# Performance work log

Hardware: AMD Instinct MI355X
Metric: run time of the kernel (lower is better)

## Reference

```python
import jax, jax.numpy as jnp
import numpy as np

N, D, H = 4096, 1024, 8
DH = D // H
EPS = 1e-5


def layer_norm(x, g, b):
    mu = jnp.mean(x, axis=-1, keepdims=True)
    var = jnp.mean(jnp.square(x - mu), axis=-1, keepdims=True)
    return (x - mu) * jax.lax.rsqrt(var + EPS) * g + b


def setup_inputs() -> dict:
    key = jax.random.key(0)
    ks = jax.random.split(key, 12)
    s = 0.02
    inp = {
        "x": jax.random.normal(ks[0], (N, D), dtype=jnp.float32),
        "adj": (jax.random.uniform(ks[1], (N, N)) < 0.01).astype(jnp.float32),
        "Wq": jax.random.normal(ks[2], (D, D), dtype=jnp.float32) * s,
        "Wk": jax.random.normal(ks[3], (D, D), dtype=jnp.float32) * s,
        "Wv": jax.random.normal(ks[4], (D, D), dtype=jnp.float32) * s,
        "Wo_w": jax.random.normal(ks[5], (D, D), dtype=jnp.float32) * s,
        "Wo_b": jnp.zeros((D,), dtype=jnp.float32),
        "adj_bias": jnp.full((H,), 1.0, dtype=jnp.float32),
        "ln1_g": jnp.ones((D,), dtype=jnp.float32),
        "ln1_b": jnp.zeros((D,), dtype=jnp.float32),
        "ffn_ln_g": jnp.ones((D,), dtype=jnp.float32),
        "ffn_ln_b": jnp.zeros((D,), dtype=jnp.float32),
        "ffn_w1": jax.random.normal(ks[6], (D, 2 * D), dtype=jnp.float32) * s,
        "ffn_b1": jnp.zeros((2 * D,), dtype=jnp.float32),
        "ffn_w2": jax.random.normal(ks[7], (2 * D, D), dtype=jnp.float32) * s,
        "ffn_b2": jnp.zeros((D,), dtype=jnp.float32),
    }
    return inp


def reference(x, adj, Wq, Wk, Wv, Wo_w, Wo_b, adj_bias, ln1_g, ln1_b,
              ffn_ln_g, ffn_ln_b, ffn_w1, ffn_b1, ffn_w2, ffn_b2):
    scale = DH ** -0.5
    Q = (x @ Wq).reshape(N, H, DH)
    K = (x @ Wk).reshape(N, H, DH)
    V = (x @ Wv).reshape(N, H, DH)
    # attn[i,h,j] = <Q_i, K_j> * scale + beta_h * adj[i,j]
    attn = jnp.einsum('bhd,nhd->bhn', Q, K) * scale
    attn = attn + adj_bias[None, :, None] * adj[:, None, :]
    attn = jax.nn.softmax(attn, axis=-1)  # dropout in eval mode -> identity
    out = jnp.einsum('bhn,nhd->bhd', attn, V).reshape(N, D)
    out = out @ Wo_w + Wo_b
    h = layer_norm(x + out, ln1_g, ln1_b)
    f = layer_norm(h, ffn_ln_g, ffn_ln_b)
    f = jax.nn.gelu(f @ ffn_w1 + ffn_b1, approximate=False) @ ffn_w2 + ffn_b2
    return h + f
```

## Files before the change

kernel.cpp:

```cpp
#include <hip/hip_runtime.h>
#include <hip/hip_bf16.h>
#include <cstdint>
#include <cstddef>

typedef __hip_bfloat16 bf16;
typedef __attribute__((ext_vector_type(8))) short short8;
typedef __attribute__((ext_vector_type(4))) short short4v;
typedef __attribute__((ext_vector_type(4))) float floatx4;
typedef unsigned long long u64;

#define DEVI static __device__ __forceinline__

DEVI void load_lds16(const void* g, void* l) {
  __builtin_amdgcn_global_load_lds((const __attribute__((address_space(1))) unsigned int*)g,
                                   (__attribute__((address_space(3))) unsigned int*)l, 16, 0, 0);
}
DEVI short8 ld8(const bf16* p) { return *(const short8*)p; }
DEVI floatx4 mfma16(short8 a, short8 b, floatx4 c) {
  return __builtin_amdgcn_mfma_f32_16x16x32_bf16(a, b, c, 0, 0, 0);
}
DEVI short bfb(float f) { bf16 h = __float2bfloat16(f); return __builtin_bit_cast(short, h); }
DEVI float fbf(short s) { bf16 h = __builtin_bit_cast(bf16, s); return __bfloat162float(h); }

__global__ __launch_bounds__(256)
void prep_kernel(const float* __restrict__ x, bf16* __restrict__ xb,
                 const float* __restrict__ adj, u64* __restrict__ bits) {
  const int row = blockIdx.x, tid = threadIdx.x;
  const int wave = tid >> 6, lane = tid & 63;
  float4 v = ((const float4*)(x + (size_t)row * 1024))[tid];
  bf16* o = xb + (size_t)row * 1024 + tid * 4;
  o[0] = __float2bfloat16(v.x); o[1] = __float2bfloat16(v.y);
  o[2] = __float2bfloat16(v.z); o[3] = __float2bfloat16(v.w);
  const float* arow = adj + (size_t)row * 4096;
#pragma unroll
  for (int it = 0; it < 16; it++) {
    int col = it * 256 + tid;
    u64 m = __ballot(arow[col] != 0.f);
    if (lane == 0) bits[(size_t)row * 64 + it * 4 + wave] = m;
  }
}

DEVI void tr_tile(const float* in, bf16* out, int R, int C, int bx, int by) {
  __shared__ float t[32][33];
  int c0 = bx * 32, r0 = by * 32;
  int tx = threadIdx.x, ty = threadIdx.y;
#pragma unroll
  for (int i = 0; i < 32; i += 8) t[ty + i][tx] = in[(size_t)(r0 + ty + i) * C + c0 + tx];
  __syncthreads();
#pragma unroll
  for (int i = 0; i < 32; i += 8)
    out[(size_t)(c0 + ty + i) * R + r0 + tx] = __float2bfloat16(t[tx][ty + i]);
}

__global__ __launch_bounds__(256)
void tr_all(const float* Wq, const float* Wk, const float* Wv, const float* Wo,
            const float* W1, const float* W2,
            bf16* Wqkvt, bf16* Wot, bf16* W1t, bf16* W2t) {
  int id = blockIdx.x;
  if (id < 4096) {
    int w = id >> 10, t = id & 1023;
    const float* in = w == 0 ? Wq : w == 1 ? Wk : w == 2 ? Wv : Wo;
    bf16* out = w == 0 ? Wqkvt : w == 1 ? Wqkvt + 1024ull * 1024
                : w == 2 ? Wqkvt + 2048ull * 1024 : Wot;
    tr_tile(in, out, 1024, 1024, t & 31, t >> 5);
  } else if (id < 6144) {
    int t = id - 4096;
    tr_tile(W1, W1t, 1024, 2048, t & 63, t >> 6);
  } else {
    int t = id - 6144;
    tr_tile(W2, W2t, 2048, 1024, t & 31, t >> 5);
  }
}

__global__ __launch_bounds__(256)
void tr_bf16p(const bf16* __restrict__ in, bf16* __restrict__ out, int inLd) {
  __shared__ bf16 t[32][33];
  int c0 = blockIdx.x * 32, r0 = blockIdx.y * 32;
  int tx = threadIdx.x, ty = threadIdx.y;
#pragma unroll
  for (int i = 0; i < 32; i += 8) t[ty + i][tx] = in[(size_t)(r0 + ty + i) * inLd + c0 + tx];
  __syncthreads();
#pragma unroll
  for (int i = 0; i < 32; i += 8) {
    int k = r0 + tx;
    int pk = (k & ~63) | ((k & 15) << 2) | ((k >> 4) & 3);
    out[(size_t)(c0 + ty + i) * 4096 + pk] = t[tx][ty + i];
  }
}

template <int MODE>
__global__ __launch_bounds__(256)
void gemm_bt(const bf16* __restrict__ A, const bf16* __restrict__ Bt,
             const float* __restrict__ bias, const float* __restrict__ resid,
             float* __restrict__ outF, bf16* __restrict__ outB,
             int M, int Nn, int K) {
  __shared__ alignas(16) bf16 As[3][128 * 32];
  __shared__ alignas(16) bf16 Bs[3][128 * 32];
  const int tid = threadIdx.x;
  const int wave = tid >> 6, lane = tid & 63;
  const int m0 = blockIdx.y * 128, n0 = blockIdx.x * 128;
  const int wr = (wave >> 1) * 64, wc = (wave & 1) * 64;
  const int l15 = lane & 15, qq = lane >> 4;
  const int lr = lane >> 2, l4 = lane & 3;
  const int Kspan = K / gridDim.z;
  const int kbeg = blockIdx.z * Kspan;
  const int T = Kspan >> 5;

  floatx4 acc[4][4];
#pragma unroll
  for (int i = 0; i < 4; i++)
#pragma unroll
    for (int j = 0; j < 4; j++) acc[i][j] = (floatx4)0.f;

  const bf16* gA0 = A + (size_t)(m0 + wave * 16 + lr) * K + kbeg + l4 * 8;
  const bf16* gA1 = gA0 + (size_t)64 * K;
  const bf16* gB0 = Bt + (size_t)(n0 + wave * 16 + lr) * K + kbeg + l4 * 8;
  const bf16* gB1 = gB0 + (size_t)64 * K;
  const int lo = wave * 16 * 32;

  auto stage = [&](int t, int buf) {
    int kt = t * 32;
    load_lds16(gA0 + kt, &As[buf][lo]);
    load_lds16(gA1 + kt, &As[buf][64 * 32 + lo]);
    load_lds16(gB0 + kt, &Bs[buf][lo]);
    load_lds16(gB1 + kt, &Bs[buf][64 * 32 + lo]);
  };
  stage(0, 0);
  stage(1, 1);

  int bc = 0;
  for (int t = 0; t < T; ++t) {
    if (t < T - 1) asm volatile("s_waitcnt vmcnt(4) lgkmcnt(0)" ::: "memory");
    else           asm volatile("s_waitcnt vmcnt(0) lgkmcnt(0)" ::: "memory");
    __builtin_amdgcn_s_barrier();
    if (t + 2 < T) { int bs = bc == 0 ? 2 : bc - 1; stage(t + 2, bs); }

    short8 af[4], bfr[4];
#pragma unroll
    for (int mi = 0; mi < 4; mi++) af[mi] = ld8(&As[bc][(wr + mi * 16 + l15) * 32 + qq * 8]);
#pragma unroll
    for (int ni = 0; ni < 4; ni++) bfr[ni] = ld8(&Bs[bc][(wc + ni * 16 + l15) * 32 + qq * 8]);
#pragma unroll
    for (int mi = 0; mi < 4; mi++)
#pragma unroll
      for (int ni = 0; ni < 4; ni++)
        acc[mi][ni] = mfma16(af[mi], bfr[ni], acc[mi][ni]);
    bc = bc == 2 ? 0 : bc + 1;
  }

  const size_t zoff = (size_t)blockIdx.z * M * Nn;
#pragma unroll
  for (int mi = 0; mi < 4; mi++) {
    int row = m0 + wr + mi * 16 + qq * 4;
#pragma unroll
    for (int ni = 0; ni < 4; ni++) {
      int col = n0 + wc + ni * 16 + l15;
      float bv = 0.f;
      if (MODE == 2) bv = bias[col];
      if (MODE == 4 && blockIdx.z == 0) bv = bias[col];
#pragma unroll
      for (int r = 0; r < 4; r++) {
        float v = acc[mi][ni][r] + bv;
        size_t off = (size_t)(row + r) * Nn + col;
        if (MODE == 0) {
          outB[off] = __float2bfloat16(v);
        } else if (MODE == 2) {
          outB[off] = __float2bfloat16(0.5f * v * (1.f + erff(v * 0.70710678118654752f)));
        } else {
          if (resid && blockIdx.z == 1) v += resid[off];
          outF[zoff + off] = v;
        }
      }
    }
  }
}

__global__ __launch_bounds__(256, 3)
void attn_kernel(const bf16* __restrict__ QKV, const bf16* __restrict__ Vtp,
                 const u64* __restrict__ adjbits, const float* __restrict__ adj_bias,
                 bf16* __restrict__ AOpart, float* __restrict__ lpart) {
  __shared__ alignas(16) bf16 Kf[16 * 512];
  __shared__ alignas(16) bf16 Vf[16 * 512];
  __shared__ alignas(16) bf16 Ps[4][32 * 68];
  const int q0 = blockIdx.x * 128;
  const int h = blockIdx.y;
  const int split = blockIdx.z;
  const int k0 = split * 1024;
  const int tid = threadIdx.x, wave = tid >> 6, lane = tid & 63;
  const int l15 = lane & 15, qq = lane >> 4;
  const float beta = adj_bias[h];
  const float scale = 0.08838834764831845f;

  short8 qf[2][4];
#pragma unroll
  for (int mi = 0; mi < 2; mi++)
#pragma unroll
    for (int kk = 0; kk < 4; kk++)
      qf[mi][kk] = ld8(&QKV[(size_t)(q0 + wave * 32 + mi * 16 + l15) * 3072 +
                            h * 128 + kk * 32 + qq * 8]);

  floatx4 o[2][8];
#pragma unroll
  for (int mi = 0; mi < 2; mi++)
#pragma unroll
    for (int ni = 0; ni < 8; ni++) o[mi][ni] = (floatx4)0.f;
  float lrow[2][4];
#pragma unroll
  for (int mi = 0; mi < 2; mi++)
#pragma unroll
    for (int r = 0; r < 4; r++) lrow[mi][r] = 0.f;

  bf16* PsW = &Ps[wave][0];

  short8 kpre[4], vpre[4];
  u64 abc[2][4], abn[2][4];
  auto fetchK = [&](int kt, short8* dst) {
#pragma unroll
    for (int i = 0; i < 4; i++) {
      int fi = wave * 4 + i, ni = fi >> 2, kk = fi & 3;
      dst[i] = ld8(&QKV[(size_t)(kt + ni * 16 + l15) * 3072 + 1024 +
                        h * 128 + kk * 32 + qq * 8]);
    }
  };
  auto fetchV = [&](int kt, short8* dst) {
#pragma unroll
    for (int i = 0; i < 4; i++) {
      int fi = wave * 4 + i, ni = fi >> 1, kk = fi & 1;
      dst[i] = ld8(&Vtp[(size_t)(h * 128 + ni * 16 + l15) * 4096 + kt + kk * 32 + qq * 8]);
    }
  };
  auto fetchA = [&](int t, u64 (*ab)[4]) {
#pragma unroll
    for (int mi = 0; mi < 2; mi++)
#pragma unroll
      for (int r = 0; r < 4; r++)
        ab[mi][r] = adjbits[(size_t)(q0 + wave * 32 + mi * 16 + qq * 4 + r) * 64 +
                            split * 16 + t];
  };
  fetchK(k0, kpre);
  fetchV(k0, vpre);
  fetchA(0, abc);

  for (int t = 0; t < 16; t++) {
    const int kt = k0 + t * 64;
    __syncthreads();
#pragma unroll
    for (int i = 0; i < 4; i++) {
      *(short8*)&Kf[(wave * 4 + i) * 512 + lane * 8] = kpre[i];
      *(short8*)&Vf[(wave * 4 + i) * 512 + lane * 8] = vpre[i];
    }
    __syncthreads();
    if (t < 15) { fetchK(kt + 64, kpre); fetchV(kt + 64, vpre); fetchA(t + 1, abn); }

#pragma unroll
    for (int mi = 0; mi < 2; mi++) {
      floatx4 s[4];
#pragma unroll
      for (int ni = 0; ni < 4; ni++) s[ni] = (floatx4)0.f;
#pragma unroll
      for (int kk = 0; kk < 4; kk++) {
#pragma unroll
        for (int ni = 0; ni < 4; ni++) {
          short8 kf = ld8(&Kf[(ni * 4 + kk) * 512 + lane * 8]);
          s[ni] = mfma16(qf[mi][kk], kf, s[ni]);
        }
      }
#pragma unroll
      for (int r = 0; r < 4; r++) {
        u64 bits = abc[mi][r];
        unsigned lo = (unsigned)(bits >> l15);
        unsigned hi = (unsigned)(bits >> (l15 + 32));
        float b0 = (lo & 1u) ? beta : 0.f;
        float b1 = (lo & 0x10000u) ? beta : 0.f;
        float b2 = (hi & 1u) ? beta : 0.f;
        float b3 = (hi & 0x10000u) ? beta : 0.f;
        float p0 = __expf(fmaf(s[0][r], scale, b0));
        float p1 = __expf(fmaf(s[1][r], scale, b1));
        float p2 = __expf(fmaf(s[2][r], scale, b2));
        float p3 = __expf(fmaf(s[3][r], scale, b3));
        lrow[mi][r] += (p0 + p1) + (p2 + p3);
        short4v pk;
        pk.x = bfb(p0); pk.y = bfb(p1); pk.z = bfb(p2); pk.w = bfb(p3);
        *(short4v*)&PsW[(mi * 16 + qq * 4 + r) * 68 + l15 * 4] = pk;
      }
    }

#pragma unroll
    for (int kk = 0; kk < 2; kk++) {
      short8 af0 = ld8(&PsW[(0 + l15) * 68 + kk * 32 + qq * 8]);
      short8 af1 = ld8(&PsW[(16 + l15) * 68 + kk * 32 + qq * 8]);
#pragma unroll
      for (int ni = 0; ni < 8; ni++) {
        short8 vf = ld8(&Vf[(ni * 2 + kk) * 512 + lane * 8]);
        o[0][ni] = mfma16(af0, vf, o[0][ni]);
        o[1][ni] = mfma16(af1, vf, o[1][ni]);
      }
    }
#pragma unroll
    for (int mi = 0; mi < 2; mi++)
#pragma unroll
      for (int r = 0; r < 4; r++) abc[mi][r] = abn[mi][r];
  }

#pragma unroll
  for (int mi = 0; mi < 2; mi++) {
#pragma unroll
    for (int r = 0; r < 4; r++) {
      float v = lrow[mi][r];
#pragma unroll
      for (int ofs = 1; ofs < 16; ofs <<= 1) v += __shfl_xor(v, ofs, 16);
      int rloc = wave * 32 + mi * 16 + qq * 4 + r;
      int grow = q0 + rloc;
      if (l15 == 0) lpart[((size_t)split * 4096 + grow) * 8 + h] = v;
      bf16* dst = AOpart + ((size_t)split * 4096 + grow) * 1024 + h * 128;
#pragma unroll
      for (int ni = 0; ni < 8; ni++) dst[ni * 16 + l15] = __float2bfloat16(o[mi][ni][r]);
    }
  }
}

__global__ __launch_bounds__(256)
void attn_norm(const bf16* __restrict__ AOpart, const float* __restrict__ lpart,
               bf16* __restrict__ AO) {
  int row = blockIdx.x, tid = threadIdx.x;
  int h = tid >> 5;
  float ls = 0.f;
#pragma unroll
  for (int s = 0; s < 4; s++) ls += lpart[((size_t)s * 4096 + row) * 8 + h];
  float a0 = 0.f, a1 = 0.f, a2 = 0.f, a3 = 0.f;
#pragma unroll
  for (int s = 0; s < 4; s++) {
    short4v v = *(const short4v*)&AOpart[((size_t)s * 4096 + row) * 1024 + tid * 4];
    a0 += fbf(v.x); a1 += fbf(v.y); a2 += fbf(v.z); a3 += fbf(v.w);
  }
  float inv = 1.f / ls;
  bf16* op = AO + (size_t)row * 1024 + tid * 4;
  op[0] = __float2bfloat16(a0 * inv);
  op[1] = __float2bfloat16(a1 * inv);
  op[2] = __float2bfloat16(a2 * inv);
  op[3] = __float2bfloat16(a3 * inv);
}

DEVI void block_sum2(float& a, float& b, float* red) {
#pragma unroll
  for (int o = 1; o < 64; o <<= 1) { a += __shfl_xor(a, o, 64); b += __shfl_xor(b, o, 64); }
  int wv = threadIdx.x >> 6;
  if ((threadIdx.x & 63) == 0) { red[wv] = a; red[4 + wv] = b; }
  __syncthreads();
  a = red[0] + red[1] + red[2] + red[3];
  b = red[4] + red[5] + red[6] + red[7];
  __syncthreads();
}

__global__ __launch_bounds__(256)
void ln2_kernel(const float* __restrict__ x, const float* __restrict__ ao0,
                const float* __restrict__ ao1,
                const float* __restrict__ g1, const float* __restrict__ b1,
                const float* __restrict__ g2, const float* __restrict__ b2,
                float* __restrict__ hout, bf16* __restrict__ fln) {
  __shared__ float red[8];
  const int row = blockIdx.x, tid = threadIdx.x;
  float4 xv = ((const float4*)(x + (size_t)row * 1024))[tid];
  float4 av = ((const float4*)(ao0 + (size_t)row * 1024))[tid];
  float4 aw = ((const float4*)(ao1 + (size_t)row * 1024))[tid];
  float s0 = xv.x + av.x + aw.x, s1 = xv.y + av.y + aw.y;
  float s2 = xv.z + av.z + aw.z, s3 = xv.w + av.w + aw.w;
  float sum = s0 + s1 + s2 + s3;
  float ssq = s0 * s0 + s1 * s1 + s2 * s2 + s3 * s3;
  block_sum2(sum, ssq, red);
  float mu = sum * (1.f / 1024.f);
  float rs = rsqrtf(ssq * (1.f / 1024.f) - mu * mu + 1e-5f);
  float4 gv = ((const float4*)g1)[tid], bv = ((const float4*)b1)[tid];
  float h0 = (s0 - mu) * rs * gv.x + bv.x;
  float h1 = (s1 - mu) * rs * gv.y + bv.y;
  float h2 = (s2 - mu) * rs * gv.z + bv.z;
  float h3 = (s3 - mu) * rs * gv.w + bv.w;
  float4 hv; hv.x = h0; hv.y = h1; hv.z = h2; hv.w = h3;
  ((float4*)(hout + (size_t)row * 1024))[tid] = hv;
  float sum2 = h0 + h1 + h2 + h3;
  float ssq2 = h0 * h0 + h1 * h1 + h2 * h2 + h3 * h3;
  block_sum2(sum2, ssq2, red);
  float mu2 = sum2 * (1.f / 1024.f);
  float rs2 = rsqrtf(ssq2 * (1.f / 1024.f) - mu2 * mu2 + 1e-5f);
  float4 g2v = ((const float4*)g2)[tid], b2v = ((const float4*)b2)[tid];
  bf16* op = fln + (size_t)row * 1024 + tid * 4;
  op[0] = __float2bfloat16((h0 - mu2) * rs2 * g2v.x + b2v.x);
  op[1] = __float2bfloat16((h1 - mu2) * rs2 * g2v.y + b2v.y);
  op[2] = __float2bfloat16((h2 - mu2) * rs2 * g2v.z + b2v.z);
  op[3] = __float2bfloat16((h3 - mu2) * rs2 * g2v.w + b2v.w);
}

__global__ __launch_bounds__(256)
void add2_kernel(const float* __restrict__ a, const float* __restrict__ b,
                 float* __restrict__ o) {
  int i = blockIdx.x * 256 + threadIdx.x;
  float4 va = ((const float4*)a)[i];
  float4 vb = ((const float4*)b)[i];
  float4 vo; vo.x = va.x + vb.x; vo.y = va.y + vb.y;
  vo.z = va.z + vb.z; vo.w = va.w + vb.w;
  ((float4*)o)[i] = vo;
}

extern "C" void kernel_launch(void* const* d_in, const int* in_sizes, int n_in,
                              void* d_out, int out_size, void* d_ws, size_t ws_size,
                              hipStream_t stream) {
  const float* x    = (const float*)d_in[0];
  const float* adj  = (const float*)d_in[1];
  const float* Wq   = (const float*)d_in[2];
  const float* Wk   = (const float*)d_in[3];
  const float* Wv   = (const float*)d_in[4];
  const float* Wo   = (const float*)d_in[5];
  const float* Wob  = (const float*)d_in[6];
  const float* adjb = (const float*)d_in[7];
  const float* g1   = (const float*)d_in[8];
  const float* b1   = (const float*)d_in[9];
  const float* g2   = (const float*)d_in[10];
  const float* b2   = (const float*)d_in[11];
  const float* W1   = (const float*)d_in[12];
  const float* fb1  = (const float*)d_in[13];
  const float* W2   = (const float*)d_in[14];
  const float* fb2  = (const float*)d_in[15];
  float* out = (float*)d_out;

  char* w = (char*)d_ws;
  size_t off = 0;
  auto take = [&](size_t bytes) {
    char* p = w + off;
    off += (bytes + 255) & ~(size_t)255;
    return p;
  };
  bf16* xb    = (bf16*)take(4096ull * 1024 * 2);
  bf16* Wqkvt = (bf16*)take(3072ull * 1024 * 2);
  bf16* Wot   = (bf16*)take(1024ull * 1024 * 2);
  bf16* W1t   = (bf16*)take(2048ull * 1024 * 2);
  bf16* W2t   = (bf16*)take(1024ull * 2048 * 2);
  bf16* QKV   = (bf16*)take(4096ull * 3072 * 2);
  bf16* Vtp   = (bf16*)take(1024ull * 4096 * 2);
  bf16* AO    = (bf16*)take(4096ull * 1024 * 2);
  u64*  adjbits = (u64*)take(4096ull * 64 * 8);
  float* lpart  = (float*)take(4ull * 4096 * 8 * 4);
  char* big = take(32ull << 20);
  bf16*  AOpart = (bf16*)big;
  float* WoP    = (float*)big;
  float* F2P    = (float*)big;
  float* H   = (float*)take(4096ull * 1024 * 4);
  bf16*  FLN = (bf16*)take(4096ull * 1024 * 2);
  bf16*  G   = (bf16*)take(4096ull * 2048 * 2);

  dim3 tb(32, 8);
  prep_kernel<<<4096, 256, 0, stream>>>(x, xb, adj, adjbits);
  tr_all<<<8192, tb, 0, stream>>>(Wq, Wk, Wv, Wo, W1, W2, Wqkvt, Wot, W1t, W2t);

  gemm_bt<0><<<dim3(24, 32, 1), 256, 0, stream>>>(xb, Wqkvt, nullptr, nullptr,
                                                  nullptr, QKV, 4096, 3072, 1024);
  tr_bf16p<<<dim3(32, 128), tb, 0, stream>>>(QKV + 2048, Vtp, 3072);
  attn_kernel<<<dim3(32, 8, 4), 256, 0, stream>>>(QKV, Vtp, adjbits, adjb, AOpart, lpart);
  attn_norm<<<4096, 256, 0, stream>>>(AOpart, lpart, AO);
  gemm_bt<4><<<dim3(8, 32, 2), 256, 0, stream>>>(AO, Wot, Wob, nullptr,
                                                 WoP, nullptr, 4096, 1024, 1024);
  ln2_kernel<<<4096, 256, 0, stream>>>(x, WoP, WoP + 4096ull * 1024, g1, b1, g2, b2, H, FLN);
  gemm_bt<2><<<dim3(16, 32, 1), 256, 0, stream>>>(FLN, W1t, fb1, nullptr,
                                                  nullptr, G, 4096, 2048, 1024);
  gemm_bt<4><<<dim3(8, 32, 2), 256, 0, stream>>>(G, W2t, fb2, H,
                                                 F2P, nullptr, 4096, 1024, 2048);
  add2_kernel<<<4096, 256, 0, stream>>>(F2P, F2P + 4096ull * 1024, out);
}
```

Measured before the change: 491.2 us.

## Preload adjacency bitmask tile into LDS and interleave QK MFMAs across row tiles

Loads the block's whole adjacency bitmask slice (128 rows x 16 words) into shared memory once at kernel start, replacing the per-iteration register double-buffered global fetches. The QK^T MFMA loop is restructured so both row sub-tiles share each K fragment load from LDS, which halves K fragment reads. Occupancy hint drops from 3 to 2 blocks per CU to allow more registers for the larger score accumulator set, at the cost of fewer resident waves for latency hiding. The upfront 16KB LDS also raises shared memory use per block.

```diff
diff --git a/kernel.cpp b/kernel.cpp
--- a/kernel.cpp
+++ b/kernel.cpp
@@ -175,13 +175,14 @@
   }
 }
 
-__global__ __launch_bounds__(256, 3)
+__global__ __launch_bounds__(256, 2)
 void attn_kernel(const bf16* __restrict__ QKV, const bf16* __restrict__ Vtp,
                  const u64* __restrict__ adjbits, const float* __restrict__ adj_bias,
                  bf16* __restrict__ AOpart, float* __restrict__ lpart) {
   __shared__ alignas(16) bf16 Kf[16 * 512];
   __shared__ alignas(16) bf16 Vf[16 * 512];
   __shared__ alignas(16) bf16 Ps[4][32 * 68];
+  __shared__ u64 Abits[128 * 16];
   const int q0 = blockIdx.x * 128;
   const int h = blockIdx.y;
   const int split = blockIdx.z;
@@ -191,6 +192,12 @@
   const float beta = adj_bias[h];
   const float scale = 0.08838834764831845f;
 
+#pragma unroll
+  for (int i = 0; i < 8; i++) {
+    int idx = tid + i * 256;
+    Abits[idx] = adjbits[(size_t)(q0 + (idx >> 4)) * 64 + split * 16 + (idx & 15)];
+  }
+
   short8 qf[2][4];
 #pragma unroll
   for (int mi = 0; mi < 2; mi++)
@@ -213,7 +220,6 @@
   bf16* PsW = &Ps[wave][0];
 
   short8 kpre[4], vpre[4];
-  u64 abc[2][4], abn[2][4];
   auto fetchK = [&](int kt, short8* dst) {
 #pragma unroll
     for (int i = 0; i < 4; i++) {
@@ -229,17 +235,8 @@
       dst[i] = ld8(&Vtp[(size_t)(h * 128 + ni * 16 + l15) * 4096 + kt + kk * 32 + qq * 8]);
     }
   };
-  auto fetchA = [&](int t, u64 (*ab)[4]) {
-#pragma unroll
-    for (int mi = 0; mi < 2; mi++)
-#pragma unroll
-      for (int r = 0; r < 4; r++)
-        ab[mi][r] = adjbits[(size_t)(q0 + wave * 32 + mi * 16 + qq * 4 + r) * 64 +
-                            split * 16 + t];
-  };
   fetchK(k0, kpre);
   fetchV(k0, vpre);
-  fetchA(0, abc);
 
   for (int t = 0; t < 16; t++) {
     const int kt = k0 + t * 64;
@@ -250,34 +247,39 @@
       *(short8*)&Vf[(wave * 4 + i) * 512 + lane * 8] = vpre[i];
     }
     __syncthreads();
-    if (t < 15) { fetchK(kt + 64, kpre); fetchV(kt + 64, vpre); fetchA(t + 1, abn); }
+    if (t < 15) { fetchK(kt + 64, kpre); fetchV(kt + 64, vpre); }
+
+    floatx4 s[2][4];
+#pragma unroll
+    for (int mi = 0; mi < 2; mi++)
+#pragma unroll
+      for (int ni = 0; ni < 4; ni++) s[mi][ni] = (floatx4)0.f;
+#pragma unroll
+    for (int kk = 0; kk < 4; kk++) {
+#pragma unroll
+      for (int ni = 0; ni < 4; ni++) {
+        short8 kf = ld8(&Kf[(ni * 4 + kk) * 512 + lane * 8]);
+        s[0][ni] = mfma16(qf[0][kk], kf, s[0][ni]);
+        s[1][ni] = mfma16(qf[1][kk], kf, s[1][ni]);
+      }
+    }
 
 #pragma unroll
     for (int mi = 0; mi < 2; mi++) {
-      floatx4 s[4];
-#pragma unroll
-      for (int ni = 0; ni < 4; ni++) s[ni] = (floatx4)0.f;
-#pragma unroll
-      for (int kk = 0; kk < 4; kk++) {
-#pragma unroll
-        for (int ni = 0; ni < 4; ni++) {
-          short8 kf = ld8(&Kf[(ni * 4 + kk) * 512 + lane * 8]);
-          s[ni] = mfma16(qf[mi][kk], kf, s[ni]);
-        }
-      }
 #pragma unroll
       for (int r = 0; r < 4; r++) {
-        u64 bits = abc[mi][r];
+        int rloc = wave * 32 + mi * 16 + qq * 4 + r;
+        u64 bits = Abits[rloc * 16 + t];
         unsigned lo = (unsigned)(bits >> l15);
         unsigned hi = (unsigned)(bits >> (l15 + 32));
         float b0 = (lo & 1u) ? beta : 0.f;
         float b1 = (lo & 0x10000u) ? beta : 0.f;
         float b2 = (hi & 1u) ? beta : 0.f;
         float b3 = (hi & 0x10000u) ? beta : 0.f;
-        float p0 = __expf(fmaf(s[0][r], scale, b0));
-        float p1 = __expf(fmaf(s[1][r], scale, b1));
-        float p2 = __expf(fmaf(s[2][r], scale, b2));
-        float p3 = __expf(fmaf(s[3][r], scale, b3));
+        float p0 = __expf(fmaf(s[mi][0][r], scale, b0));
+        float p1 = __expf(fmaf(s[mi][1][r], scale, b1));
+        float p2 = __expf(fmaf(s[mi][2][r], scale, b2));
+        float p3 = __expf(fmaf(s[mi][3][r], scale, b3));
         lrow[mi][r] += (p0 + p1) + (p2 + p3);
         short4v pk;
         pk.x = bfb(p0); pk.y = bfb(p1); pk.z = bfb(p2); pk.w = bfb(p3);
@@ -296,10 +298,6 @@
         o[1][ni] = mfma16(af1, vf, o[1][ni]);
       }
     }
-#pragma unroll
-    for (int mi = 0; mi < 2; mi++)
-#pragma unroll
-      for (int r = 0; r < 4; r++) abc[mi][r] = abn[mi][r];
   }
 
 #pragma unroll
```

After: 461.7 us. 1.06x faster.
